# Kernel optimization log

Hardware: AMD Instinct MI355X
Metric: run time of the kernel (lower is better)

Reference implementation:

```python
import jax, jax.numpy as jnp
import numpy as np

EMBED_DIM = 1024
NUM_HEADS = 16
HEAD_DIM = EMBED_DIM // NUM_HEADS
SEQ_LEN = 4096


def setup_inputs() -> dict:
    key = jax.random.key(0)
    kx, kq, kk, kv = jax.random.split(key, 4)
    x = jax.random.normal(kx, (SEQ_LEN, EMBED_DIM), dtype=jnp.float32)
    Wq = jax.random.normal(kq, (EMBED_DIM, EMBED_DIM), dtype=jnp.float32)
    Wk = jax.random.normal(kk, (EMBED_DIM, EMBED_DIM), dtype=jnp.float32)
    Wv = jax.random.normal(kv, (EMBED_DIM, EMBED_DIM), dtype=jnp.float32)
    return {"x": x, "Wq": Wq, "Wk": Wk, "Wv": Wv}


def reference(x, Wq, Wk, Wv):
    seq_len, embed_dim = x.shape
    h, d = NUM_HEADS, HEAD_DIM
    # project then split heads: [S, E] -> [H, S, D]
    q = (x @ Wq).reshape(seq_len, h, d).transpose(1, 0, 2)
    k = (x @ Wk).reshape(seq_len, h, d).transpose(1, 0, 2)
    v = (x @ Wv).reshape(seq_len, h, d).transpose(1, 0, 2)
    # full [H, S, S] scores, scaled by sqrt(head_dim) (faithful to original)
    scores = jnp.einsum("hsd,htd->hst", q, k) / jnp.sqrt(jnp.asarray(d, dtype=q.dtype))
    weights = jax.nn.softmax(scores, axis=-1)
    out = jnp.einsum("hst,htd->hsd", weights, v)  # [H, S, D]
    return out.transpose(1, 0, 2).reshape(seq_len, embed_dim)
```

## Files before the change

### kernel.cpp

```cpp
#include <hip/hip_runtime.h>
#include <hip/hip_bf16.h>

#define SEQ 4096
#define EMB 1024
#define NHD 16
#define HDD 64

using bf16 = __hip_bfloat16;
using bf16x8 = __attribute__((ext_vector_type(8))) short;
using f32x4  = __attribute__((ext_vector_type(4))) float;

#define MFMA16(a, b, c) __builtin_amdgcn_mfma_f32_16x16x32_bf16((a), (b), (c), 0, 0, 0)

#define QSCALE 0.1803368801111204f

__device__ __forceinline__ float b2f(bf16 b) { return __bfloat162float(b); }

__device__ __forceinline__ void gll16(const void* g, void* l) {
    __builtin_amdgcn_global_load_lds(
        (const __attribute__((address_space(1))) unsigned int*)g,
        (__attribute__((address_space(3))) unsigned int*)l, 16, 0, 0);
}

__global__ void split_kernel(const float* __restrict__ src, bf16* __restrict__ hi,
                             bf16* __restrict__ lo, int n4) {
    int i = blockIdx.x * blockDim.x + threadIdx.x;
    if (i >= n4) return;
    float4 v = ((const float4*)src)[i];
    float vv[4] = {v.x, v.y, v.z, v.w};
#pragma unroll
    for (int j = 0; j < 4; j++) {
        bf16 h = __float2bfloat16(vv[j]);
        hi[i * 4 + j] = h;
        lo[i * 4 + j] = __float2bfloat16(vv[j] - b2f(h));
    }
}

__global__ void wtrans_kernel(const float* __restrict__ Wq, const float* __restrict__ Wk,
                              const float* __restrict__ Wv,
                              bf16* __restrict__ thq, bf16* __restrict__ tlq,
                              bf16* __restrict__ thk, bf16* __restrict__ tlk,
                              bf16* __restrict__ thv, bf16* __restrict__ tlv) {
    __shared__ float tile[32][33];
    const float* W;
    bf16 *wth, *wtl;
    if (blockIdx.z == 0) { W = Wq; wth = thq; wtl = tlq; }
    else if (blockIdx.z == 1) { W = Wk; wth = thk; wtl = tlk; }
    else { W = Wv; wth = thv; wtl = tlv; }
    int n0 = blockIdx.x * 32, k0 = blockIdx.y * 32;
    int tx = threadIdx.x, ty = threadIdx.y;
    for (int r = ty; r < 32; r += 8)
        tile[r][tx] = W[(k0 + r) * EMB + n0 + tx];
    __syncthreads();
    for (int r = ty; r < 32; r += 8) {
        float v = tile[tx][r];
        bf16 h = __float2bfloat16(v);
        wth[(n0 + r) * EMB + k0 + tx] = h;
        wtl[(n0 + r) * EMB + k0 + tx] = __float2bfloat16(v - b2f(h));
    }
}

template <int NTERMS>
__device__ __forceinline__ void proj_loop(
    const bf16* __restrict__ Ah, const bf16* __restrict__ Al,
    const bf16* __restrict__ Bth, const bf16* __restrict__ Btl,
    bf16* lAh, bf16* lAl, bf16* lBh, bf16* lBl,
    int m0, int n0, int t, f32x4 (&acc)[4][4]) {
    const int wid = t >> 6, lane = t & 63, lr = lane & 15, lg = lane >> 4;
    const int wr = (wid >> 1) * 64, wc = (wid & 1) * 64;
    for (int k0 = 0; k0 < EMB; k0 += 32) {
#pragma unroll
        for (int c = t; c < 512; c += 256) {
            int row = c >> 2, slot = c & 3;
            *(uint4*)&lAh[row * 40 + slot * 8] =
                *(const uint4*)&Ah[(m0 + row) * EMB + k0 + slot * 8];
            *(uint4*)&lBh[row * 40 + slot * 8] =
                *(const uint4*)&Bth[(n0 + row) * EMB + k0 + slot * 8];
            if constexpr (NTERMS == 3) {
                *(uint4*)&lAl[row * 40 + slot * 8] =
                    *(const uint4*)&Al[(m0 + row) * EMB + k0 + slot * 8];
                *(uint4*)&lBl[row * 40 + slot * 8] =
                    *(const uint4*)&Btl[(n0 + row) * EMB + k0 + slot * 8];
            }
        }
        __syncthreads();
        bf16x8 fah[4], fbh[4], fal[4], fbl[4];
#pragma unroll
        for (int i = 0; i < 4; i++) {
            fah[i] = *(const bf16x8*)&lAh[(wr + i * 16 + lr) * 40 + lg * 8];
            fbh[i] = *(const bf16x8*)&lBh[(wc + i * 16 + lr) * 40 + lg * 8];
            if constexpr (NTERMS == 3) {
                fal[i] = *(const bf16x8*)&lAl[(wr + i * 16 + lr) * 40 + lg * 8];
                fbl[i] = *(const bf16x8*)&lBl[(wc + i * 16 + lr) * 40 + lg * 8];
            }
        }
#pragma unroll
        for (int i = 0; i < 4; i++)
#pragma unroll
            for (int j = 0; j < 4; j++) {
                acc[i][j] = MFMA16(fah[i], fbh[j], acc[i][j]);
                if constexpr (NTERMS == 3) {
                    acc[i][j] = MFMA16(fah[i], fbl[j], acc[i][j]);
                    acc[i][j] = MFMA16(fal[i], fbh[j], acc[i][j]);
                }
            }
        __syncthreads();
    }
}

__global__ __launch_bounds__(256) void proj_qkv(
    const bf16* __restrict__ xh, const bf16* __restrict__ xl,
    const bf16* __restrict__ thq, const bf16* __restrict__ tlq,
    const bf16* __restrict__ thk, const bf16* __restrict__ tlk,
    const bf16* __restrict__ thv,
    bf16* __restrict__ qh, bf16* __restrict__ ql,
    bf16* __restrict__ kh, bf16* __restrict__ kl, bf16* __restrict__ vt) {
    __shared__ __align__(16) bf16 lAh[128 * 40];
    __shared__ __align__(16) bf16 lAl[128 * 40];
    __shared__ __align__(16) bf16 lBh[128 * 40];
    __shared__ __align__(16) bf16 lBl[128 * 40];
    const int t = threadIdx.x;
    const int m0 = blockIdx.y * 128;
    const int which = blockIdx.x >> 3;
    const int n0 = (blockIdx.x & 7) * 128;

    f32x4 acc[4][4];
#pragma unroll
    for (int i = 0; i < 4; i++)
#pragma unroll
        for (int j = 0; j < 4; j++) acc[i][j] = (f32x4){0.f, 0.f, 0.f, 0.f};

    if (which == 0)
        proj_loop<3>(xh, xl, thq, tlq, lAh, lAl, lBh, lBl, m0, n0, t, acc);
    else if (which == 1)
        proj_loop<3>(xh, xl, thk, tlk, lAh, lAl, lBh, lBl, m0, n0, t, acc);
    else
        proj_loop<1>(xh, xl, thv, nullptr, lAh, lAl, lBh, lBl, m0, n0, t, acc);

    const int wid = t >> 6, lane = t & 63, lr = lane & 15, lg = lane >> 4;
    const int wr = (wid >> 1) * 64, wc = (wid & 1) * 64;

    if (which == 2) {
#pragma unroll
        for (int i = 0; i < 4; i++)
#pragma unroll
            for (int j = 0; j < 4; j++) {
                int n = n0 + wc + j * 16 + lr;
                int m = m0 + wr + i * 16 + lg * 4;
                __hip_bfloat162 p01 = __float22bfloat162_rn(
                    make_float2(acc[i][j][0], acc[i][j][1]));
                __hip_bfloat162 p23 = __float22bfloat162_rn(
                    make_float2(acc[i][j][2], acc[i][j][3]));
                uint2 w;
                w.x = *(unsigned int*)&p01;
                w.y = *(unsigned int*)&p23;
                *(uint2*)&vt[(size_t)n * SEQ + m] = w;
            }
    } else {
        float scale = (which == 0) ? QSCALE : 1.0f;
        bf16* Chi = (which == 0) ? qh : kh;
        bf16* Clo = (which == 0) ? ql : kl;
#pragma unroll
        for (int i = 0; i < 4; i++)
#pragma unroll
            for (int j = 0; j < 4; j++)
#pragma unroll
                for (int q = 0; q < 4; q++) {
                    float cv = acc[i][j][q] * scale;
                    int m = m0 + wr + i * 16 + lg * 4 + q;
                    int n = n0 + wc + j * 16 + lr;
                    bf16 hv = __float2bfloat16(cv);
                    Chi[m * EMB + n] = hv;
                    Clo[m * EMB + n] = __float2bfloat16(cv - b2f(hv));
                }
    }
}

__global__ __launch_bounds__(256, 4) void attn_kernel(
    const bf16* __restrict__ qh, const bf16* __restrict__ ql,
    const bf16* __restrict__ kh, const bf16* __restrict__ kl,
    const bf16* __restrict__ vt, float* __restrict__ out) {
    __shared__ __align__(16) bf16 lKh[64 * 64];
    __shared__ __align__(16) bf16 lKl[64 * 64];
    __shared__ __align__(16) bf16 lV[64 * 64];
    __shared__ __align__(16) bf16 lP[4][16 * 64];
    const int t = threadIdx.x;
    const int q0 = blockIdx.x * 64;
    const int h = blockIdx.y;
    const int wid = t >> 6, lane = t & 63, lr = lane & 15, lg = lane >> 4;
    const int wq = wid * 16;

    const bf16* qrh = qh + (size_t)(q0 + wq + lr) * EMB + h * HDD;
    const bf16* qrl = ql + (size_t)(q0 + wq + lr) * EMB + h * HDD;
    bf16x8 fqh[2], fql[2];
#pragma unroll
    for (int hf = 0; hf < 2; hf++) {
        fqh[hf] = *(const bf16x8*)(qrh + hf * 32 + lg * 8);
        fql[hf] = *(const bf16x8*)(qrl + hf * 32 + lg * 8);
    }

    const int srow = lane >> 3, slot = lane & 7;
    const char* gp[6];
    bf16* lp[6];
#pragma unroll
    for (int i = 0; i < 6; i++) {
        int cid = wid + i * 4;
        int sect = cid & 7;
        int r = sect * 8 + srow;
        int sb = (slot ^ (r & 7)) * 16;
        if (i < 2) {
            gp[i] = (const char*)kh + ((size_t)r * EMB + h * HDD) * 2 + sb;
            lp[i] = lKh + sect * 512;
        } else if (i < 4) {
            gp[i] = (const char*)kl + ((size_t)r * EMB + h * HDD) * 2 + sb;
            lp[i] = lKl + sect * 512;
        } else {
            gp[i] = (const char*)vt + ((size_t)(h * HDD + r) * SEQ) * 2 + sb;
            lp[i] = lV + sect * 512;
        }
    }

    f32x4 Ofr[4];
#pragma unroll
    for (int d = 0; d < 4; d++) Ofr[d] = (f32x4){0.f, 0.f, 0.f, 0.f};
    float Mr = -1e30f, Lr = 0.f;

    for (int s0 = 0; s0 < SEQ; s0 += 64) {
        __syncthreads();
#pragma unroll
        for (int i = 0; i < 6; i++) {
            gll16(gp[i], lp[i]);
            gp[i] += (i < 4) ? (size_t)(64 * EMB * 2) : (size_t)(64 * 2);
        }
        __syncthreads();

        __builtin_amdgcn_s_setprio(1);
        f32x4 sfr[4];
#pragma unroll
        for (int kc = 0; kc < 4; kc++) {
            int row = kc * 16 + lr;
            const char* rbh = (const char*)lKh + row * 128;
            const char* rbl = (const char*)lKl + row * 128;
            f32x4 a = (f32x4){0.f, 0.f, 0.f, 0.f};
#pragma unroll
            for (int hf = 0; hf < 2; hf++) {
                int off = (hf * 64 + lg * 16) ^ ((row & 7) << 4);
                bf16x8 kbh = *(const bf16x8*)(rbh + off);
                bf16x8 kbl = *(const bf16x8*)(rbl + off);
                a = MFMA16(kbh, fqh[hf], a);
                a = MFMA16(kbh, fql[hf], a);
                a = MFMA16(kbl, fqh[hf], a);
            }
            sfr[kc] = a;
        }
        __builtin_amdgcn_s_setprio(0);

        float mx = sfr[0][0];
#pragma unroll
        for (int kc = 0; kc < 4; kc++)
#pragma unroll
            for (int j = 0; j < 4; j++) mx = fmaxf(mx, sfr[kc][j]);
        mx = fmaxf(mx, __shfl_xor(mx, 16));
        mx = fmaxf(mx, __shfl_xor(mx, 32));

        bool resc = !__all(mx <= Mr + 11.5f);
        float mn = resc ? fmaxf(Mr, mx) : Mr;
        float ps = 0.f;
#pragma unroll
        for (int kc = 0; kc < 4; kc++)
#pragma unroll
            for (int j = 0; j < 4; j++) {
                float p = __builtin_exp2f(sfr[kc][j] - mn);
                sfr[kc][j] = p;
                ps += p;
            }
        ps += __shfl_xor(ps, 16);
        ps += __shfl_xor(ps, 32);
        if (resc) {
            float fac = __builtin_exp2f(Mr - mn);
            Mr = mn;
            Lr = Lr * fac + ps;
#pragma unroll
            for (int d = 0; d < 4; d++)
#pragma unroll
                for (int j = 0; j < 4; j++) Ofr[d][j] *= fac;
        } else {
            Lr += ps;
        }

        {
            char* pw = (char*)&lP[wid][0] + lr * 128;
#pragma unroll
            for (int kc = 0; kc < 4; kc++) {
                __hip_bfloat162 p01 =
                    __float22bfloat162_rn(make_float2(sfr[kc][0], sfr[kc][1]));
                __hip_bfloat162 p23 =
                    __float22bfloat162_rn(make_float2(sfr[kc][2], sfr[kc][3]));
                uint2 w;
                w.x = *(unsigned int*)&p01;
                w.y = *(unsigned int*)&p23;
                *(uint2*)(pw + ((kc * 32 + lg * 8) ^ ((lr & 7) << 4))) = w;
            }
        }

        __builtin_amdgcn_s_setprio(1);
#pragma unroll
        for (int ks = 0; ks < 2; ks++) {
            const char* pb = (const char*)&lP[wid][0] + lr * 128 +
                             ((ks * 64 + lg * 16) ^ ((lr & 7) << 4));
            bf16x8 pf = *(const bf16x8*)pb;
#pragma unroll
            for (int df = 0; df < 4; df++) {
                int vrow = df * 16 + lr;
                const char* pv = (const char*)lV + vrow * 128 +
                                 ((ks * 64 + lg * 16) ^ ((vrow & 7) << 4));
                bf16x8 vf = *(const bf16x8*)pv;
                Ofr[df] = MFMA16(vf, pf, Ofr[df]);
            }
        }
        __builtin_amdgcn_s_setprio(0);
    }

    float inv = 1.0f / Lr;
    float* orow = out + (size_t)(q0 + wq + lr) * EMB + h * HDD;
#pragma unroll
    for (int df = 0; df < 4; df++) {
        float4 o = make_float4(Ofr[df][0] * inv, Ofr[df][1] * inv,
                               Ofr[df][2] * inv, Ofr[df][3] * inv);
        *(float4*)(orow + df * 16 + lg * 4) = o;
    }
}

extern "C" void kernel_launch(void* const* d_in, const int* in_sizes, int n_in,
                              void* d_out, int out_size, void* d_ws, size_t ws_size,
                              hipStream_t stream) {
    const float* x = (const float*)d_in[0];
    const float* Wq = (const float*)d_in[1];
    const float* Wk = (const float*)d_in[2];
    const float* Wv = (const float*)d_in[3];
    float* out = (float*)d_out;

    char* ws = (char*)d_ws;
    size_t off = 0;
    auto alloc = [&](size_t elems) -> bf16* {
        bf16* p = (bf16*)(ws + off);
        off += elems * sizeof(bf16);
        return p;
    };
    bf16* xh = alloc((size_t)SEQ * EMB);
    bf16* xl = alloc((size_t)SEQ * EMB);
    bf16* wthq = alloc((size_t)EMB * EMB);
    bf16* wtlq = alloc((size_t)EMB * EMB);
    bf16* wthk = alloc((size_t)EMB * EMB);
    bf16* wtlk = alloc((size_t)EMB * EMB);
    bf16* wthv = alloc((size_t)EMB * EMB);
    bf16* wtlv = alloc((size_t)EMB * EMB);
    bf16* qh = alloc((size_t)SEQ * EMB);
    bf16* ql = alloc((size_t)SEQ * EMB);
    bf16* kh = alloc((size_t)SEQ * EMB);
    bf16* kl = alloc((size_t)SEQ * EMB);
    bf16* vt = alloc((size_t)SEQ * EMB);
    (void)ws_size; (void)in_sizes; (void)n_in; (void)out_size;

    split_kernel<<<(SEQ * EMB / 4 + 255) / 256, 256, 0, stream>>>(x, xh, xl, SEQ * EMB / 4);
    wtrans_kernel<<<dim3(32, 32, 3), dim3(32, 8), 0, stream>>>(
        Wq, Wk, Wv, wthq, wtlq, wthk, wtlk, wthv, wtlv);
    proj_qkv<<<dim3(24, 32), 256, 0, stream>>>(
        xh, xl, wthq, wtlq, wthk, wtlk, wthv, qh, ql, kh, kl, vt);
    attn_kernel<<<dim3(SEQ / 64, NHD), 256, 0, stream>>>(qh, ql, kh, kl, vt, out);
}
```

Measured before the change: 266.9 us.

## Double-buffer K/V tiles in attention with 8-wave blocks and head-grouped block order

The attention kernel now runs 512-thread blocks covering 128 queries, so each K/V tile loaded into LDS is shared by twice as many query rows. K/V tiles are double-buffered: the next tile is prefetched with global_load_lds while the current one is computed, which cuts the barriers per iteration from two to one. A block index swizzle groups consecutive blocks by head to improve L2 reuse of K/V. LDS use per block roughly doubles to about 64KB, which limits how many blocks fit on each CU.

```diff
diff --git a/kernel.cpp b/kernel.cpp
--- a/kernel.cpp
+++ b/kernel.cpp
@@ -176,17 +176,16 @@
     }
 }
 
-__global__ __launch_bounds__(256, 4) void attn_kernel(
+__global__ __launch_bounds__(512, 4) void attn_kernel(
     const bf16* __restrict__ qh, const bf16* __restrict__ ql,
     const bf16* __restrict__ kh, const bf16* __restrict__ kl,
     const bf16* __restrict__ vt, float* __restrict__ out) {
-    __shared__ __align__(16) bf16 lKh[64 * 64];
-    __shared__ __align__(16) bf16 lKl[64 * 64];
-    __shared__ __align__(16) bf16 lV[64 * 64];
-    __shared__ __align__(16) bf16 lP[4][16 * 64];
+    __shared__ __align__(16) bf16 lKV[2][3][64 * 64];
+    __shared__ __align__(16) bf16 lP[8][16 * 64];
     const int t = threadIdx.x;
-    const int q0 = blockIdx.x * 64;
-    const int h = blockIdx.y;
+    const int swz = (blockIdx.x & 7) * 64 + (blockIdx.x >> 3);
+    const int h = swz >> 5;
+    const int q0 = (swz & 31) * 128;
     const int wid = t >> 6, lane = t & 63, lr = lane & 15, lg = lane >> 4;
     const int wq = wid * 16;
 
@@ -200,47 +199,48 @@
     }
 
     const int srow = lane >> 3, slot = lane & 7;
-    const char* gp[6];
-    bf16* lp[6];
-#pragma unroll
-    for (int i = 0; i < 6; i++) {
-        int cid = wid + i * 4;
-        int sect = cid & 7;
-        int r = sect * 8 + srow;
-        int sb = (slot ^ (r & 7)) * 16;
-        if (i < 2) {
-            gp[i] = (const char*)kh + ((size_t)r * EMB + h * HDD) * 2 + sb;
-            lp[i] = lKh + sect * 512;
-        } else if (i < 4) {
-            gp[i] = (const char*)kl + ((size_t)r * EMB + h * HDD) * 2 + sb;
-            lp[i] = lKl + sect * 512;
-        } else {
-            gp[i] = (const char*)vt + ((size_t)(h * HDD + r) * SEQ) * 2 + sb;
-            lp[i] = lV + sect * 512;
-        }
-    }
+    const int r = wid * 8 + srow;
+    const int sb = (slot ^ (r & 7)) * 16;
+    const char* gp[3];
+    gp[0] = (const char*)kh + ((size_t)r * EMB + h * HDD) * 2 + sb;
+    gp[1] = (const char*)kl + ((size_t)r * EMB + h * HDD) * 2 + sb;
+    gp[2] = (const char*)vt + ((size_t)(h * HDD + r) * SEQ) * 2 + sb;
+    bf16* lp[3];
+#pragma unroll
+    for (int i = 0; i < 3; i++) lp[i] = &lKV[0][i][wid * 512];
 
     f32x4 Ofr[4];
 #pragma unroll
     for (int d = 0; d < 4; d++) Ofr[d] = (f32x4){0.f, 0.f, 0.f, 0.f};
     float Mr = -1e30f, Lr = 0.f;
 
-    for (int s0 = 0; s0 < SEQ; s0 += 64) {
-        __syncthreads();
-#pragma unroll
-        for (int i = 0; i < 6; i++) {
-            gll16(gp[i], lp[i]);
-            gp[i] += (i < 4) ? (size_t)(64 * EMB * 2) : (size_t)(64 * 2);
-        }
-        __syncthreads();
+#pragma unroll
+    for (int i = 0; i < 3; i++) {
+        gll16(gp[i], lp[i]);
+        gp[i] += (i < 2) ? (size_t)(64 * EMB * 2) : (size_t)(64 * 2);
+    }
+    __syncthreads();
+
+    for (int tk = 0; tk < SEQ / 64; tk++) {
+        const int cur = tk & 1;
+        if (tk < SEQ / 64 - 1) {
+#pragma unroll
+            for (int i = 0; i < 3; i++) {
+                gll16(gp[i], lp[i] + (cur ^ 1) * 12288);
+                gp[i] += (i < 2) ? (size_t)(64 * EMB * 2) : (size_t)(64 * 2);
+            }
+        }
+        const char* cKh = (const char*)&lKV[cur][0][0];
+        const char* cKl = (const char*)&lKV[cur][1][0];
+        const char* cV  = (const char*)&lKV[cur][2][0];
 
         __builtin_amdgcn_s_setprio(1);
         f32x4 sfr[4];
 #pragma unroll
         for (int kc = 0; kc < 4; kc++) {
             int row = kc * 16 + lr;
-            const char* rbh = (const char*)lKh + row * 128;
-            const char* rbl = (const char*)lKl + row * 128;
+            const char* rbh = cKh + row * 128;
+            const char* rbl = cKl + row * 128;
             f32x4 a = (f32x4){0.f, 0.f, 0.f, 0.f};
 #pragma unroll
             for (int hf = 0; hf < 2; hf++) {
@@ -312,13 +312,15 @@
 #pragma unroll
             for (int df = 0; df < 4; df++) {
                 int vrow = df * 16 + lr;
-                const char* pv = (const char*)lV + vrow * 128 +
+                const char* pv = cV + vrow * 128 +
                                  ((ks * 64 + lg * 16) ^ ((vrow & 7) << 4));
                 bf16x8 vf = *(const bf16x8*)pv;
                 Ofr[df] = MFMA16(vf, pf, Ofr[df]);
             }
         }
         __builtin_amdgcn_s_setprio(0);
+
+        __syncthreads();
     }
 
     float inv = 1.0f / Lr;
@@ -367,5 +369,5 @@
         Wq, Wk, Wv, wthq, wtlq, wthk, wtlk, wthv, wtlv);
     proj_qkv<<<dim3(24, 32), 256, 0, stream>>>(
         xh, xl, wthq, wtlq, wthk, wtlk, wthv, qh, ql, kh, kl, vt);
-    attn_kernel<<<dim3(SEQ / 64, NHD), 256, 0, stream>>>(qh, ql, kh, kl, vt, out);
-}
+    attn_kernel<<<512, 512, 0, stream>>>(qh, ql, kh, kl, vt, out);
+}
```

After: 251.2 us. -5.9%, faster.
